# Performance work log

Measured on AMD Instinct MI355X. Metric: run time of the kernel, lower is better.

The kernel has to match this reference:

```python
import jax, jax.numpy as jnp
import numpy as np

N_NODES = 50000
N_EDGES = 1600000
D_IN = 128
D_OUT = 32
N_HEADS = 4


def setup_inputs() -> dict:
    key = jax.random.key(0)
    k1, k2, k3, k4 = jax.random.split(key, 4)
    x = jax.random.normal(k1, (N_NODES, D_IN), dtype=jnp.float32)
    edge_index = jax.random.randint(k2, (2, N_EDGES), 0, N_NODES, dtype=jnp.int64)
    W = jax.random.normal(k3, (N_HEADS, D_IN, D_OUT), dtype=jnp.float32) * 0.01
    a = jax.random.normal(k4, (N_HEADS, 2 * D_OUT), dtype=jnp.float32) * 0.01
    return {"x": x, "edge_index": edge_index, "W": W, "a": a}


def reference(x, edge_index, W, a):
    N = x.shape[0]
    K, d_in, d_out = W.shape
    # Per-head projected node features: [N, K, d_out]
    Wh = jnp.einsum('ni,kio->nko', x, W)
    src, tgt = edge_index[0], edge_index[1]
    # cat([Wh[src], Wh[tgt]]) . a  ==  Wh[src].a[:, :d] + Wh[tgt].a[:, d:]
    s_src = jnp.einsum('nkd,kd->nk', Wh, a[:, :d_out])  # [N, K]
    s_tgt = jnp.einsum('nkd,kd->nk', Wh, a[:, d_out:])  # [N, K]
    e = s_src[src] + s_tgt[tgt]                          # [E, K]
    e = jnp.where(e > 0, e, 0.2 * e)                     # LeakyReLU(0.2)
    # Segment-softmax over incoming edges of each target node
    e_max = jax.ops.segment_max(e, tgt, num_segments=N)  # [N, K], -inf for empty
    e_max = jnp.where(jnp.isfinite(e_max), e_max, 0.0)
    e_exp = jnp.exp(e - e_max[tgt])                      # [E, K]
    e_sum = jax.ops.segment_sum(e_exp, tgt, num_segments=N)  # [N, K]
    alpha = e_exp / (e_sum[tgt] + 1e-10)                 # [E, K]
    # Weighted scatter-add aggregation: [N, K, d_out]
    weighted = alpha[:, :, None] * Wh[src]
    out = jax.ops.segment_sum(weighted, tgt, num_segments=N)
    out = out.reshape(N, K * d_out)
    return jnp.where(out > 0, out, jnp.expm1(out))       # ELU
```

## Files before the change

kernel.cpp:

```cpp
#include <hip/hip_runtime.h>
#include <math.h>

#define N_HEADS 4
#define D_IN    128
#define D_OUT   32
#define D_TOT   128
#define TN      64
#define XPAD    132
#define BSH     6
#define BNODES  64
#define MAXNB   1024
#define EPT     16
#define CAP     2560

static __device__ __forceinline__ unsigned short f2bf(float f) {
    unsigned u = __float_as_uint(f);
    u += 0x7fffu + ((u >> 16) & 1u);
    return (unsigned short)(u >> 16);
}

__global__ __launch_bounds__(256) void front_kernel(
    const float* __restrict__ x,
    const float* __restrict__ W,
    const float* __restrict__ a,
    const int*  __restrict__ ei,
    int*  __restrict__ cursor,
    unsigned int* __restrict__ bbuf,
    unsigned int* __restrict__ Whu,
    float* __restrict__ s_src,
    float* __restrict__ s_tgt,
    int N, int E, int nProj, int nb) {

    __shared__ float xs[TN][XPAD];
    const int t = threadIdx.x;

    if (blockIdx.x >= nProj) {
        int* cnt = (int*)xs;
        for (int i = t; i < nb; i += 256) cnt[i] = 0;
        __syncthreads();

        const int e0 = (blockIdx.x - nProj) * (256 * EPT);
        int src[EPT], tgt[EPT];
        #pragma unroll
        for (int i = 0; i < EPT; ++i) {
            int e = e0 + i * 256 + t;
            if (e < E) {
                src[i] = ei[e];
                tgt[i] = ei[E + e];
                atomicAdd(&cnt[tgt[i] >> BSH], 1);
            } else {
                src[i] = -1; tgt[i] = 0;
            }
        }
        __syncthreads();
        for (int b = t; b < nb; b += 256)
            if (cnt[b]) cnt[b] = atomicAdd(&cursor[b], cnt[b]);
        __syncthreads();
        #pragma unroll
        for (int i = 0; i < EPT; ++i) {
            if (src[i] >= 0) {
                int b = tgt[i] >> BSH;
                int pos = atomicAdd(&cnt[b], 1);
                if (pos < CAP)
                    bbuf[(size_t)b * CAP + pos] =
                        ((unsigned)(tgt[i] & (BNODES - 1)) << 16) | (unsigned)src[i];
            }
        }
        return;
    }

    const int n0 = blockIdx.x * TN;
    {
        const int r  = t >> 2;
        const int c0 = (t & 3) * 32;
        int nn = n0 + r; if (nn >= N) nn = N - 1;
        const float4* src = (const float4*)(x + (size_t)nn * D_IN + c0);
        #pragma unroll
        for (int j = 0; j < 8; ++j)
            *(float4*)&xs[r][c0 + j * 4] = src[j];
    }
    __syncthreads();

    const int fg = t & 15;
    const int ng = t >> 4;
    const int f0 = fg * 8;
    const int k  = f0 >> 5;
    const int o0 = f0 & 31;
    const float* Wf = W + k * (D_IN * D_OUT) + o0;

    float acc[4][8];
    #pragma unroll
    for (int nl = 0; nl < 4; ++nl)
        #pragma unroll
        for (int j = 0; j < 8; ++j) acc[nl][j] = 0.f;

    #pragma unroll 2
    for (int i = 0; i < D_IN; i += 4) {
        float4 wa[4], wb[4];
        #pragma unroll
        for (int ii = 0; ii < 4; ++ii) {
            wa[ii] = *(const float4*)(Wf + (i + ii) * D_OUT);
            wb[ii] = *(const float4*)(Wf + (i + ii) * D_OUT + 4);
        }
        #pragma unroll
        for (int nl = 0; nl < 4; ++nl) {
            const float4 xv = *(const float4*)&xs[ng * 4 + nl][i];
            const float xr[4] = {xv.x, xv.y, xv.z, xv.w};
            #pragma unroll
            for (int ii = 0; ii < 4; ++ii) {
                acc[nl][0] = fmaf(xr[ii], wa[ii].x, acc[nl][0]);
                acc[nl][1] = fmaf(xr[ii], wa[ii].y, acc[nl][1]);
                acc[nl][2] = fmaf(xr[ii], wa[ii].z, acc[nl][2]);
                acc[nl][3] = fmaf(xr[ii], wa[ii].w, acc[nl][3]);
                acc[nl][4] = fmaf(xr[ii], wb[ii].x, acc[nl][4]);
                acc[nl][5] = fmaf(xr[ii], wb[ii].y, acc[nl][5]);
                acc[nl][6] = fmaf(xr[ii], wb[ii].z, acc[nl][6]);
                acc[nl][7] = fmaf(xr[ii], wb[ii].w, acc[nl][7]);
            }
        }
    }

    const float4 as0 = *(const float4*)(a + k * (2 * D_OUT) + o0);
    const float4 as1 = *(const float4*)(a + k * (2 * D_OUT) + o0 + 4);
    const float4 at0 = *(const float4*)(a + k * (2 * D_OUT) + D_OUT + o0);
    const float4 at1 = *(const float4*)(a + k * (2 * D_OUT) + D_OUT + o0 + 4);

    #pragma unroll
    for (int nl = 0; nl < 4; ++nl) {
        const int n = n0 + ng * 4 + nl;
        if (n < N) {
            unsigned int p[4];
            #pragma unroll
            for (int j = 0; j < 4; ++j)
                p[j] = (unsigned)f2bf(acc[nl][2 * j]) |
                       ((unsigned)f2bf(acc[nl][2 * j + 1]) << 16);
            *(uint4*)&Whu[(size_t)n * 64 + fg * 4] = make_uint4(p[0], p[1], p[2], p[3]);

            float vs = acc[nl][0] * as0.x + acc[nl][1] * as0.y +
                       acc[nl][2] * as0.z + acc[nl][3] * as0.w +
                       acc[nl][4] * as1.x + acc[nl][5] * as1.y +
                       acc[nl][6] * as1.z + acc[nl][7] * as1.w;
            float vt = acc[nl][0] * at0.x + acc[nl][1] * at0.y +
                       acc[nl][2] * at0.z + acc[nl][3] * at0.w +
                       acc[nl][4] * at1.x + acc[nl][5] * at1.y +
                       acc[nl][6] * at1.z + acc[nl][7] * at1.w;
            vs += __shfl_xor(vs, 1, 64); vs += __shfl_xor(vs, 2, 64);
            vt += __shfl_xor(vt, 1, 64); vt += __shfl_xor(vt, 2, 64);
            if ((fg & 3) == 0) {
                s_src[n * N_HEADS + k] = vs;
                s_tgt[n * N_HEADS + k] = vt;
            }
        }
    }
}

__global__ __launch_bounds__(256) void finalize_kernel(
    const unsigned int* __restrict__ bbuf,
    const int* __restrict__ cursor,
    int* __restrict__ rs_beg,
    int* __restrict__ rs_end,
    unsigned short* __restrict__ rec,
    int N) {

    __shared__ int hist[BNODES];
    __shared__ int cur[BNODES];
    const int b = blockIdx.x;
    const int t = threadIdx.x;
    const int cnt = cursor[b];
    const int base = b * CAP;

    if (t < BNODES) hist[t] = 0;
    __syncthreads();
    for (int j = t; j < cnt; j += 256)
        atomicAdd(&hist[bbuf[base + j] >> 16], 1);
    __syncthreads();

    if (t < BNODES) {
        int v = hist[t];
        int incl = v;
        #pragma unroll
        for (int off = 1; off < 64; off <<= 1) {
            int tv = __shfl_up(incl, off, 64);
            if (t >= off) incl += tv;
        }
        int excl = incl - v;
        cur[t] = excl;
        int n = b * BNODES + t;
        if (n < N) {
            rs_beg[n] = base + excl;
            rs_end[n] = base + excl + v;
        }
    }
    __syncthreads();

    for (int j = t; j < cnt; j += 256) {
        unsigned v = bbuf[base + j];
        int pos = atomicAdd(&cur[v >> 16], 1);
        rec[base + pos] = (unsigned short)(v & 0xFFFFu);
    }
}

__global__ __launch_bounds__(256) void agg_kernel(
    const unsigned short* __restrict__ rec,
    const int* __restrict__ rs_beg,
    const int* __restrict__ rs_end,
    const float* __restrict__ s_src,
    const float* __restrict__ s_tgt,
    const unsigned int* __restrict__ Whu,
    float* __restrict__ out, int N) {

    const int n = blockIdx.x * 4 + (threadIdx.x >> 6);
    if (n >= N) return;
    const int t    = threadIdx.x & 63;
    const int k    = t >> 4;
    const int i16  = t & 15;
    const int srcl = t & 48;

    const int beg = rs_beg[n];
    const int end = rs_end[n];
    const float stk = s_tgt[(n << 2) + k];

    float den = 0.f, nx = 0.f, ny = 0.f;
    for (int j = beg; j < end; j += 16) {
        const int m = (end - j < 16) ? (end - j) : 16;
        float ev = 0.f;
        int   sv = 0;
        if (i16 < m) {
            sv = rec[j + i16];
            float av = s_src[(sv << 2) + k] + stk;
            av = av > 0.f ? av : 0.2f * av;
            ev = __expf(av);
        }
        den += ev;

        if (m == 16) {
            #pragma unroll
            for (int ii = 0; ii < 16; ii += 4) {
                const float e0 = __shfl(ev, srcl + ii,     64);
                const float e1 = __shfl(ev, srcl + ii + 1, 64);
                const float e2 = __shfl(ev, srcl + ii + 2, 64);
                const float e3 = __shfl(ev, srcl + ii + 3, 64);
                const int   s0 = __shfl(sv, srcl + ii,     64);
                const int   s1 = __shfl(sv, srcl + ii + 1, 64);
                const int   s2 = __shfl(sv, srcl + ii + 2, 64);
                const int   s3 = __shfl(sv, srcl + ii + 3, 64);
                const unsigned w0 = Whu[((unsigned)s0 << 6) + (unsigned)t];
                const unsigned w1 = Whu[((unsigned)s1 << 6) + (unsigned)t];
                const unsigned w2 = Whu[((unsigned)s2 << 6) + (unsigned)t];
                const unsigned w3 = Whu[((unsigned)s3 << 6) + (unsigned)t];
                nx = fmaf(e0, __uint_as_float(w0 << 16), nx);
                ny = fmaf(e0, __uint_as_float(w0 & 0xffff0000u), ny);
                nx = fmaf(e1, __uint_as_float(w1 << 16), nx);
                ny = fmaf(e1, __uint_as_float(w1 & 0xffff0000u), ny);
                nx = fmaf(e2, __uint_as_float(w2 << 16), nx);
                ny = fmaf(e2, __uint_as_float(w2 & 0xffff0000u), ny);
                nx = fmaf(e3, __uint_as_float(w3 << 16), nx);
                ny = fmaf(e3, __uint_as_float(w3 & 0xffff0000u), ny);
            }
        } else {
            for (int ii = 0; ii < m; ++ii) {
                const float e0 = __shfl(ev, srcl + ii, 64);
                const int   s0 = __shfl(sv, srcl + ii, 64);
                const unsigned w0 = Whu[((unsigned)s0 << 6) + (unsigned)t];
                nx = fmaf(e0, __uint_as_float(w0 << 16), nx);
                ny = fmaf(e0, __uint_as_float(w0 & 0xffff0000u), ny);
            }
        }
    }
    den += __shfl_xor(den, 1, 64);
    den += __shfl_xor(den, 2, 64);
    den += __shfl_xor(den, 4, 64);
    den += __shfl_xor(den, 8, 64);
    const float inv = 1.f / (den + 1e-10f);
    float ox = nx * inv, oy = ny * inv;
    ox = ox > 0.f ? ox : expm1f(ox);
    oy = oy > 0.f ? oy : expm1f(oy);
    *(float2*)&out[((size_t)n << 7) + (t << 1)] = make_float2(ox, oy);
}

extern "C" void kernel_launch(void* const* d_in, const int* in_sizes, int n_in,
                              void* d_out, int out_size, void* d_ws, size_t ws_size,
                              hipStream_t stream) {
    const float* x  = (const float*)d_in[0];
    const int*   ei = (const int*)d_in[1];
    const float* W  = (const float*)d_in[2];
    const float* a  = (const float*)d_in[3];
    float* out = (float*)d_out;

    const int N = in_sizes[0] / D_IN;
    const int E = in_sizes[1] / 2;
    const int nb = (N + BNODES - 1) >> BSH;

    unsigned int* Whu = (unsigned int*)d_ws;
    float* s_src    = (float*)(Whu + (size_t)N * 64);
    float* s_tgt    = s_src + (size_t)N * N_HEADS;
    int*   cursor   = (int*)(s_tgt + (size_t)N * N_HEADS);
    int*   rs_beg   = cursor + nb;
    int*   rs_end   = rs_beg + N;
    unsigned int* bbuf = (unsigned int*)(rs_end + N);
    unsigned short* rec = (unsigned short*)(bbuf + (size_t)nb * CAP);

    hipMemsetAsync(cursor, 0, (size_t)nb * sizeof(int), stream);

    const int nProj = (N + TN - 1) / TN;
    const int nBkt  = (E + 256 * EPT - 1) / (256 * EPT);
    front_kernel<<<nProj + nBkt, 256, 0, stream>>>(
        x, W, a, ei, cursor, bbuf, Whu, s_src, s_tgt, N, E, nProj, nb);

    finalize_kernel<<<nb, 256, 0, stream>>>(bbuf, cursor, rs_beg, rs_end, rec, N);

    agg_kernel<<<(N + 3) / 4, 256, 0, stream>>>(
        rec, rs_beg, rs_end, s_src, s_tgt, Whu, out, N);
}
```

Before: 132.0 us.

## Pad per-node edge lists to even length and aggregate with uniform wave-wide edge loads

Per-node edge segments are padded to even offsets so the aggregation kernel can read source indices as 32-bit pairs. Every lane in the wave now reads the same 8 edges and computes their scores redundantly, which removes the per-chunk shuffles and the cross-lane reduction of the denominator. Node and range values are made wave-uniform with readfirstlane, and the tail is handled with masked loads clamped to the bucket. In exchange it adds redundant exp and score loads per lane and a capacity clamp that could drop edges in an overfull bucket.

```diff
diff --git a/kernel.cpp b/kernel.cpp
--- a/kernel.cpp
+++ b/kernel.cpp
@@ -177,18 +177,22 @@
 
     if (t < BNODES) {
         int v = hist[t];
-        int incl = v;
+        int vp = (v + 1) & ~1;
+        int incl = vp;
         #pragma unroll
         for (int off = 1; off < 64; off <<= 1) {
             int tv = __shfl_up(incl, off, 64);
             if (t >= off) incl += tv;
         }
-        int excl = incl - v;
+        int excl = incl - vp;
+        if (excl > CAP) excl = CAP;
+        int e2 = excl + v;
+        if (e2 > CAP) e2 = CAP;
         cur[t] = excl;
         int n = b * BNODES + t;
         if (n < N) {
             rs_beg[n] = base + excl;
-            rs_end[n] = base + excl + v;
+            rs_end[n] = base + e2;
         }
     }
     __syncthreads();
@@ -196,7 +200,8 @@
     for (int j = t; j < cnt; j += 256) {
         unsigned v = bbuf[base + j];
         int pos = atomicAdd(&cur[v >> 16], 1);
-        rec[base + pos] = (unsigned short)(v & 0xFFFFu);
+        if (pos < CAP)
+            rec[base + pos] = (unsigned short)(v & 0xFFFFu);
     }
 }
 
@@ -209,68 +214,77 @@
     const unsigned int* __restrict__ Whu,
     float* __restrict__ out, int N) {
 
-    const int n = blockIdx.x * 4 + (threadIdx.x >> 6);
+    const int nraw = blockIdx.x * 4 + (threadIdx.x >> 6);
+    const int n = __builtin_amdgcn_readfirstlane(nraw);
     if (n >= N) return;
-    const int t    = threadIdx.x & 63;
-    const int k    = t >> 4;
-    const int i16  = t & 15;
-    const int srcl = t & 48;
-
-    const int beg = rs_beg[n];
-    const int end = rs_end[n];
-    const float stk = s_tgt[(n << 2) + k];
+    const int t = threadIdx.x & 63;
+    const int k = t >> 4;
+
+    const int beg = __builtin_amdgcn_readfirstlane(rs_beg[n]);
+    const int end = __builtin_amdgcn_readfirstlane(rs_end[n]);
+
+    const float4 st4 = *(const float4*)(s_tgt + ((size_t)n << 2));
+    const float stk = (k & 2) ? ((k & 1) ? st4.w : st4.z)
+                              : ((k & 1) ? st4.y : st4.x);
+    const unsigned* rec32 = (const unsigned*)rec;
 
     float den = 0.f, nx = 0.f, ny = 0.f;
-    for (int j = beg; j < end; j += 16) {
-        const int m = (end - j < 16) ? (end - j) : 16;
-        float ev = 0.f;
-        int   sv = 0;
-        if (i16 < m) {
-            sv = rec[j + i16];
-            float av = s_src[(sv << 2) + k] + stk;
-            av = av > 0.f ? av : 0.2f * av;
-            ev = __expf(av);
-        }
-        den += ev;
-
-        if (m == 16) {
-            #pragma unroll
-            for (int ii = 0; ii < 16; ii += 4) {
-                const float e0 = __shfl(ev, srcl + ii,     64);
-                const float e1 = __shfl(ev, srcl + ii + 1, 64);
-                const float e2 = __shfl(ev, srcl + ii + 2, 64);
-                const float e3 = __shfl(ev, srcl + ii + 3, 64);
-                const int   s0 = __shfl(sv, srcl + ii,     64);
-                const int   s1 = __shfl(sv, srcl + ii + 1, 64);
-                const int   s2 = __shfl(sv, srcl + ii + 2, 64);
-                const int   s3 = __shfl(sv, srcl + ii + 3, 64);
-                const unsigned w0 = Whu[((unsigned)s0 << 6) + (unsigned)t];
-                const unsigned w1 = Whu[((unsigned)s1 << 6) + (unsigned)t];
-                const unsigned w2 = Whu[((unsigned)s2 << 6) + (unsigned)t];
-                const unsigned w3 = Whu[((unsigned)s3 << 6) + (unsigned)t];
-                nx = fmaf(e0, __uint_as_float(w0 << 16), nx);
-                ny = fmaf(e0, __uint_as_float(w0 & 0xffff0000u), ny);
-                nx = fmaf(e1, __uint_as_float(w1 << 16), nx);
-                ny = fmaf(e1, __uint_as_float(w1 & 0xffff0000u), ny);
-                nx = fmaf(e2, __uint_as_float(w2 << 16), nx);
-                ny = fmaf(e2, __uint_as_float(w2 & 0xffff0000u), ny);
-                nx = fmaf(e3, __uint_as_float(w3 << 16), nx);
-                ny = fmaf(e3, __uint_as_float(w3 & 0xffff0000u), ny);
-            }
-        } else {
-            for (int ii = 0; ii < m; ++ii) {
-                const float e0 = __shfl(ev, srcl + ii, 64);
-                const int   s0 = __shfl(sv, srcl + ii, 64);
-                const unsigned w0 = Whu[((unsigned)s0 << 6) + (unsigned)t];
-                nx = fmaf(e0, __uint_as_float(w0 << 16), nx);
-                ny = fmaf(e0, __uint_as_float(w0 & 0xffff0000u), ny);
-            }
-        }
-    }
-    den += __shfl_xor(den, 1, 64);
-    den += __shfl_xor(den, 2, 64);
-    den += __shfl_xor(den, 4, 64);
-    den += __shfl_xor(den, 8, 64);
+    int j = beg;
+    for (; j + 8 <= end; j += 8) {
+        unsigned d[4];
+        #pragma unroll
+        for (int q = 0; q < 4; ++q) d[q] = rec32[(j >> 1) + q];
+        int sv[8];
+        #pragma unroll
+        for (int q = 0; q < 4; ++q) {
+            sv[2 * q]     = (int)(d[q] & 0xFFFFu);
+            sv[2 * q + 1] = (int)(d[q] >> 16);
+        }
+        unsigned w[8];
+        float av[8];
+        #pragma unroll
+        for (int q = 0; q < 8; ++q) {
+            const float4 sq = *(const float4*)(s_src + ((size_t)sv[q] << 2));
+            av[q] = ((k & 2) ? ((k & 1) ? sq.w : sq.z)
+                             : ((k & 1) ? sq.y : sq.x)) + stk;
+            w[q] = Whu[((unsigned)sv[q] << 6) + (unsigned)t];
+        }
+        #pragma unroll
+        for (int q = 0; q < 8; ++q) {
+            float a2 = av[q] > 0.f ? av[q] : 0.2f * av[q];
+            const float ev = __expf(a2);
+            den += ev;
+            nx = fmaf(ev, __uint_as_float(w[q] << 16), nx);
+            ny = fmaf(ev, __uint_as_float(w[q] & 0xffff0000u), ny);
+        }
+    }
+    if (j < end) {
+        const int dmax = (((n >> 6) + 1) * CAP) >> 1;
+        unsigned d[4];
+        #pragma unroll
+        for (int q = 0; q < 4; ++q) {
+            int di = (j >> 1) + q;
+            d[q] = rec32[di < dmax ? di : dmax - 1];
+        }
+        const int sv0 = (int)(d[0] & 0xFFFFu);
+        #pragma unroll
+        for (int q = 0; q < 8; ++q) {
+            const bool ok = (j + q) < end;
+            int sv = (q & 1) ? (int)(d[q >> 1] >> 16)
+                             : (int)(d[q >> 1] & 0xFFFFu);
+            sv = ok ? sv : sv0;
+            const float4 sq = *(const float4*)(s_src + ((size_t)sv << 2));
+            float a2 = ((k & 2) ? ((k & 1) ? sq.w : sq.z)
+                                : ((k & 1) ? sq.y : sq.x)) + stk;
+            a2 = a2 > 0.f ? a2 : 0.2f * a2;
+            const float ev = ok ? __expf(a2) : 0.f;
+            den += ev;
+            const unsigned w = Whu[((unsigned)sv << 6) + (unsigned)t];
+            nx = fmaf(ev, __uint_as_float(w << 16), nx);
+            ny = fmaf(ev, __uint_as_float(w & 0xffff0000u), ny);
+        }
+    }
+
     const float inv = 1.f / (den + 1e-10f);
     float ox = nx * inv, oy = ny * inv;
     ox = ox > 0.f ? ox : expm1f(ox);
```

Result: slower. 169.8 us (+28.6%).
